# Kernel tuning notes

Measured on AMD Instinct MI355X. Metric: run time of the kernel, lower is better.

The kernel has to match this reference:

```python
import jax, jax.numpy as jnp
import numpy as np
import math

B, DIM, H, W = 16, 384, 64, 64
SCALES, HEADS, HID = 4, 4, 32
WIDTH = DIM // SCALES
NUMS = SCALES - 1
PH = PW = 2
LS = 1e-6


def setup_inputs():
    ks = jax.random.split(jax.random.key(0), 20)
    n = lambda i, shape, s=0.02: jax.random.normal(ks[i], shape, jnp.float32) * s
    return {
        'x': jax.random.normal(ks[0], (B, DIM, H, W), jnp.float32),
        'convs_w': n(1, (NUMS, WIDTH, 3, 3)), 'convs_b': n(2, (NUMS, WIDTH)),
        'pos_w': n(3, (DIM, 2 * HID)), 'pos_b': n(4, (DIM,)),
        'ln_xca_w': jnp.ones((DIM,), jnp.float32), 'ln_xca_b': jnp.zeros((DIM,), jnp.float32),
        'gamma_xca': jnp.full((DIM,), LS, jnp.float32),
        'xca_temp': jnp.ones((HEADS, 1, 1), jnp.float32),
        'xca_kv_w': n(5, (2 * DIM, DIM)), 'xca_kv_b': n(6, (2 * DIM,)),
        'xca_proj_w': n(7, (DIM, DIM)), 'xca_proj_b': n(8, (DIM,)),
        'conv_out_w': n(9, (DIM,)), 'conv_out_b': n(10, (DIM,)),
        'wa_kv_w': n(11, (2 * DIM, DIM)), 'wa_kv_b': n(12, (2 * DIM,)),
        'wa_proj_w': n(13, (DIM, DIM)), 'wa_proj_b': n(14, (DIM,)),
        'ln_w': jnp.ones((DIM,), jnp.float32), 'ln_b': jnp.zeros((DIM,), jnp.float32),
        'pw1_w': n(15, (4 * DIM, DIM)), 'pw1_b': n(16, (4 * DIM,)),
        'pw2_w': n(17, (DIM, 4 * DIM)), 'pw2_b': n(18, (DIM,)),
        'gamma': jnp.full((DIM,), LS, jnp.float32),
    }


def layer_norm(x, w, b, eps=1e-6):
    m = jnp.mean(x, -1, keepdims=True)
    v = jnp.mean((x - m) ** 2, -1, keepdims=True)
    return (x - m) * jax.lax.rsqrt(v + eps) * w + b


def l2norm(x, eps=1e-12):  # torch F.normalize over last dim
    return x / jnp.maximum(jnp.linalg.norm(x, axis=-1, keepdims=True), eps)


def dwconv3x3(x, w, b):  # depthwise: w [Cw,3,3]
    out = jax.lax.conv_general_dilated(x, w[:, None], (1, 1), ((1, 1), (1, 1)),
        dimension_numbers=('NCHW', 'OIHW', 'NCHW'), feature_group_count=w.shape[0])
    return out + b[None, :, None, None]


def pos_fourier(pos_w, pos_b):  # -> [H*W, DIM] (batch-independent since mask is all-false)
    scale = 2 * math.pi
    y = jnp.arange(1, H + 1, dtype=jnp.float32)[:, None] / (H + 1e-6) * scale
    xg = jnp.arange(1, W + 1, dtype=jnp.float32)[None, :] / (W + 1e-6) * scale
    y = jnp.broadcast_to(y, (H, W))
    xg = jnp.broadcast_to(xg, (H, W))
    dim_t = jnp.arange(HID, dtype=jnp.float32)
    dim_t = 10000.0 ** (2 * jnp.floor(dim_t / 2) / HID)
    px = xg[..., None] / dim_t
    py = y[..., None] / dim_t
    px = jnp.stack((jnp.sin(px[..., 0::2]), jnp.cos(px[..., 1::2])), -1).reshape(H, W, HID)
    py = jnp.stack((jnp.sin(py[..., 0::2]), jnp.cos(py[..., 1::2])), -1).reshape(H, W, HID)
    pos = jnp.concatenate((py, px), -1)  # [H,W,2*HID]
    return (pos @ pos_w.T + pos_b).reshape(H * W, DIM)


def xca_fn(x, const, kv_w, kv_b, proj_w, proj_b, temp):
    b, n, c = x.shape
    h, hd = HEADS, c // HEADS
    q1 = const.reshape(b, n, h, hd).transpose(0, 2, 3, 1)          # b,h,hd,n
    kv = (x @ kv_w.T + kv_b).reshape(b, n, 2, h, hd).transpose(2, 0, 3, 1, 4)
    k = l2norm(kv[0].transpose(0, 1, 3, 2))                        # b,h,hd,n (L2 over n)
    v = kv[1].transpose(0, 1, 3, 2)                                # b,h,hd,n
    attn = jax.nn.softmax(jnp.einsum('bhcn,bhdn->bhcd', q1, k) * temp, -1)
    out = jnp.einsum('bhcd,bhdn->bhcn', attn, v)
    out = out.transpose(0, 3, 1, 2).reshape(b, n, c)
    return out @ proj_w.T + proj_b


def window_attn(x, const, kv_w, kv_b, proj_w, proj_b):
    b, n, c = x.shape
    h, hd = HEADS, c // HEADS
    kv = (x @ kv_w.T + kv_b).reshape(b, n, 2, h, hd).transpose(2, 0, 3, 1, 4)
    k = l2norm(kv[0].transpose(0, 1, 3, 2))                        # b,h,hd,n
    v = kv[1].transpose(0, 1, 3, 2)                                # b,h,hd,n
    q1 = const.reshape(b, n, 1, h, hd).transpose(2, 0, 3, 1, 4)    # 1,b,h,n,hd (leading 1 kept, as in torch)
    q1 = q1.transpose(0, 1, 2, 4, 3)                               # 1,b,h,hd,n
    logits = jnp.einsum('obhcn,bhdn->obhcd', q1, k)
    attn = 0.5 * logits / math.sqrt(hd) + 0.5 * jax.nn.softmax(logits, -1)
    attn = jax.nn.softmax(attn, -1)
    out = jnp.einsum('obhcd,bhdn->obhcn', attn, v)                 # 1,b,h,hd,n
    out = out.transpose(0, 2, 1, 3, 4).reshape(b, n, c)            # torch .transpose(1,2).reshape(B,N,C)
    return out @ proj_w.T + proj_b


def unfold(x):  # H,W divisible by patch -> no interpolate branch
    b, c = x.shape[0], x.shape[1]
    nph, npw = H // PH, W // PW
    x = x.reshape(b * c * nph, PH, npw, PW).transpose(0, 2, 1, 3)
    x = x.reshape(b, c, nph * npw, PH * PW).transpose(0, 3, 2, 1)
    return x.reshape(b * PH * PW, nph * npw, c)


def fold(x):
    c = x.shape[-1]
    nph, npw = H // PH, W // PW
    x = x.reshape(B, PH * PW, nph * npw, c).transpose(0, 3, 2, 1)
    x = x.reshape(B * c * nph, npw, PH, PW).transpose(0, 2, 1, 3)
    return x.reshape(B, c, nph * PH, npw * PW)


def reference(x, convs_w, convs_b, pos_w, pos_b, ln_xca_w, ln_xca_b, gamma_xca,
              xca_temp, xca_kv_w, xca_kv_b, xca_proj_w, xca_proj_b,
              conv_out_w, conv_out_b, wa_kv_w, wa_kv_b, wa_proj_w, wa_proj_b,
              ln_w, ln_b, pw1_w, pw1_b, pw2_w, pw2_b, gamma):
    inp = x
    # multi-scale depthwise convs (Res2Net style)
    spx = jnp.split(x, SCALES, axis=1)
    outs = []
    sp = spx[0]
    for i in range(NUMS):
        if i > 0:
            sp = sp + spx[i]
        sp = dwconv3x3(sp, convs_w[i], convs_b[i])
        outs.append(sp)
    x = jnp.concatenate(outs + [spx[NUMS]], axis=1)
    N = H * W
    x3 = x.reshape(B, DIM, N).transpose(0, 2, 1)                   # B,N,C
    x3 = x3 + pos_fourier(pos_w, pos_b)[None]
    const = inp.reshape(B, DIM, N).transpose(0, 2, 1)
    x4 = x3 + gamma_xca * xca_fn(layer_norm(x3, ln_xca_w, ln_xca_b), const,
                                 xca_kv_w, xca_kv_b, xca_proj_w, xca_proj_b, xca_temp)
    x4 = x4.reshape(B, H, W, DIM).transpose(0, 3, 1, 2)
    # conv_out: Conv2d(dim,dim,1,groups=dim) == per-channel scale+bias
    x = x4 * conv_out_w[None, :, None, None] + conv_out_b[None, :, None, None]
    x2 = window_attn(unfold(x), unfold(inp), wa_kv_w, wa_kv_b, wa_proj_w, wa_proj_b)
    x = fold(x2).transpose(0, 2, 3, 1)                             # B,H,W,C
    x = layer_norm(x, ln_w, ln_b)
    x = jax.nn.gelu(x @ pw1_w.T + pw1_b, approximate=False)
    x = x @ pw2_w.T + pw2_b
    x = gamma * x
    return inp + x.transpose(0, 3, 1, 2)
```

## Files before the change

### kernel.cpp

```cpp
#include <hip/hip_runtime.h>
#include <math.h>

#define NBATCH 16
#define CDIM   384
#define NPIX   4096
#define HDCH   96
#define NROWS  65536
#define KVHALF 25165824

typedef unsigned short bf16;
typedef __attribute__((ext_vector_type(8))) short short8;
typedef __attribute__((ext_vector_type(4))) float floatx4;

union S8U { short8 v; bf16 u[8]; };

__device__ __forceinline__ float b2f(bf16 u) {
    union { unsigned int i; float f; } c; c.i = ((unsigned int)u) << 16; return c.f;
}
__device__ __forceinline__ bf16 f2b(float f) {
    union { float f; unsigned int i; } c; c.f = f;
    unsigned int r = (c.i + 0x7FFFu + ((c.i >> 16) & 1u)) >> 16;
    return (bf16)r;
}

__device__ __forceinline__ void gload16(const bf16* g, bf16* l) {
    __builtin_amdgcn_global_load_lds(
        (const __attribute__((address_space(1))) unsigned int*)g,
        (__attribute__((address_space(3))) unsigned int*)l, 16, 0, 0);
}

__global__ __launch_bounds__(256) void zero_kernel(float* __restrict__ p) {
    p[blockIdx.x * 256 + threadIdx.x] = 0.0f;
}

__global__ __launch_bounds__(256) void wcvt_kernel(const float* __restrict__ w,
                                                   bf16* __restrict__ o, int n4) {
    int i = blockIdx.x * 256 + threadIdx.x;
    if (i < n4) {
        float4 v = ((const float4*)w)[i];
        ushort4 u;
        u.x = f2b(v.x); u.y = f2b(v.y); u.z = f2b(v.z); u.w = f2b(v.w);
        ((ushort4*)o)[i] = u;
    }
}

__global__ __launch_bounds__(128) void pos_kernel(const float* __restrict__ pos_w,
                                                  const float* __restrict__ pos_b,
                                                  bf16* __restrict__ pos) {
    __shared__ float feat[64];
    int n = blockIdx.x;
    int yi = n >> 6, xi = n & 63;
    int tid = threadIdx.x;
    if (tid < 64) {
        int j = tid & 31;
        int isx = tid >= 32;
        float base = (float)((isx ? xi : yi) + 1);
        float val = base / (64.0f + 1e-6f) * 6.283185307179586f;
        float e = (float)(2 * (j >> 1)) / 32.0f;
        float dt = powf(10000.0f, e);
        float a = val / dt;
        feat[isx * 32 + j] = (j & 1) ? cosf(a) : sinf(a);
    }
    __syncthreads();
    for (int c = tid; c < CDIM; c += 128) {
        float s = pos_b[c];
        const float* wr = pos_w + c * 64;
        #pragma unroll 16
        for (int j = 0; j < 64; ++j) s += feat[j] * wr[j];
        pos[n * CDIM + c] = f2b(s);
    }
}

__global__ __launch_bounds__(256) void dwconv_kernel(const float* __restrict__ xin, int in_ch0,
                                                     const bf16* __restrict__ prev, int prev_ch0,
                                                     const float* __restrict__ w,
                                                     const float* __restrict__ bias,
                                                     bf16* __restrict__ out, int out_ch0) {
    __shared__ float tile[66][66];
    int b = blockIdx.x / 96, c = blockIdx.x % 96;
    const float* ip = xin + (b * CDIM + in_ch0 + c) * NPIX;
    const bf16* pp = prev ? prev + (b * CDIM + prev_ch0 + c) * NPIX : nullptr;
    int tid = threadIdx.x;
    for (int i = tid; i < 66 * 66; i += 256) {
        int yy = i / 66 - 1, xx = i % 66 - 1;
        float v = 0.0f;
        if (yy >= 0 && yy < 64 && xx >= 0 && xx < 64) {
            v = ip[yy * 64 + xx];
            if (pp) v += b2f(pp[yy * 64 + xx]);
        }
        tile[i / 66][i % 66] = v;
    }
    __syncthreads();
    float wc[9];
    #pragma unroll
    for (int j = 0; j < 9; ++j) wc[j] = w[c * 9 + j];
    float b0 = bias[c];
    bf16* op = out + (b * CDIM + out_ch0 + c) * NPIX;
    for (int p = tid; p < NPIX; p += 256) {
        int y = p >> 6, x = p & 63;
        float a = b0;
        #pragma unroll
        for (int dy = 0; dy < 3; ++dy)
            #pragma unroll
            for (int dx = 0; dx < 3; ++dx)
                a += tile[y + dy][x + dx] * wc[dy * 3 + dx];
        op[p] = f2b(a);
    }
}

__global__ __launch_bounds__(256) void convert_last_kernel(const float* __restrict__ x,
                                                           bf16* __restrict__ xcat) {
    int idx = blockIdx.x * 256 + threadIdx.x;
    int b = idx / (96 * 1024);
    int rem = idx % (96 * 1024);
    const float4* src = (const float4*)(x + (b * CDIM + 288) * NPIX);
    float4 v = src[rem];
    ushort4 o;
    o.x = f2b(v.x); o.y = f2b(v.y); o.z = f2b(v.z); o.w = f2b(v.w);
    ((ushort4*)(xcat + (b * CDIM + 288) * NPIX))[rem] = o;
}

__global__ void x3_kernel(const bf16* __restrict__ xcat, const bf16* __restrict__ pos,
                          bf16* __restrict__ x3) {
    __shared__ float t[32][33];
    int c0 = blockIdx.x * 32, n0 = blockIdx.y * 32, b = blockIdx.z;
    int tx = threadIdx.x, ty = threadIdx.y;
    #pragma unroll
    for (int k = 0; k < 4; ++k) {
        int cl = ty + k * 8;
        t[cl][tx] = b2f(xcat[(b * CDIM + c0 + cl) * NPIX + n0 + tx]);
    }
    __syncthreads();
    #pragma unroll
    for (int k = 0; k < 4; ++k) {
        int nl = ty + k * 8;
        x3[(b * NPIX + n0 + nl) * CDIM + c0 + tx] =
            f2b(t[tx][nl] + b2f(pos[(n0 + nl) * CDIM + c0 + tx]));
    }
}

__global__ __launch_bounds__(128) void ln_kernel(const bf16* __restrict__ in,
                                                 const float* __restrict__ w,
                                                 const float* __restrict__ b,
                                                 bf16* __restrict__ out, int map) {
    int r = blockIdx.x;
    int src = r;
    if (map == 1) {
        int bb = r >> 12;
        int p = r & 4095;
        int y = p >> 6, x = p & 63;
        int patch = ((y & 1) << 1) | (x & 1);
        int blk = ((y >> 1) << 5) | (x >> 1);
        src = ((bb << 2) + patch) * 1024 + blk;
    }
    const bf16* row = in + src * CDIM;
    int tid = threadIdx.x;
    float v[3];
    float s1 = 0.0f, s2 = 0.0f;
    #pragma unroll
    for (int i = 0; i < 3; ++i) {
        v[i] = b2f(row[tid + i * 128]);
        s1 += v[i];
        s2 += v[i] * v[i];
    }
    __shared__ float r1[128], r2[128];
    r1[tid] = s1; r2[tid] = s2;
    __syncthreads();
    for (int off = 64; off > 0; off >>= 1) {
        if (tid < off) { r1[tid] += r1[tid + off]; r2[tid] += r2[tid + off]; }
        __syncthreads();
    }
    float mean = r1[0] * (1.0f / 384.0f);
    float var = fmaxf(r2[0] * (1.0f / 384.0f) - mean * mean, 0.0f);
    float rstd = rsqrtf(var + 1e-6f);
    #pragma unroll
    for (int i = 0; i < 3; ++i) {
        int c = tid + i * 128;
        out[r * CDIM + c] = f2b((v[i] - mean) * rstd * w[c] + b[c]);
    }
}

__global__ __launch_bounds__(256) void mfma_gemm_kernel(const bf16* __restrict__ A,
                                                        const bf16* __restrict__ W,
                                                        const float* __restrict__ bias,
                                                        bf16* __restrict__ C,
                                                        int M, int Nout, int K, int mode,
                                                        const bf16* __restrict__ res,
                                                        const float* __restrict__ scalevec,
                                                        int nlog2,
                                                        float* __restrict__ knsq_out) {
    __shared__ bf16 As[3][128][32];
    __shared__ bf16 Bs[3][128][32];
    int nx = gridDim.x, ny = gridDim.y;
    int d = blockIdx.x + nx * blockIdx.y;
    int nwg = nx * ny;
    int xt, yt;
    if ((nwg & 7) == 0) {
        int cpx = nwg >> 3;
        int wg = (d & 7) * cpx + (d >> 3);
        xt = wg / ny;
        yt = wg % ny;
    } else {
        xt = blockIdx.x; yt = blockIdx.y;
    }
    int m0 = xt * 128;
    int n0 = yt * 128;
    int tid = threadIdx.x;
    int wave = tid >> 6, lane = tid & 63;
    int wm = (wave & 1) * 64;
    int wn = (wave >> 1) * 64;
    int quad = lane >> 4;
    int lrow = lane & 15;

    int p0b = wave * 1024 + lane * 16;
    int o0 = p0b ^ (((p0b >> 7) & 3) << 4);
    int r0 = o0 >> 6;
    int ch0 = (o0 >> 4) & 3;

    const bf16* aSrc0 = A + (size_t)(m0 + r0) * K + ch0 * 8;
    const bf16* aSrc1 = A + (size_t)(m0 + r0 + 64) * K + ch0 * 8;
    const bf16* bSrc0 = W + (size_t)(n0 + r0) * K + ch0 * 8;
    const bf16* bSrc1 = W + (size_t)(n0 + r0 + 64) * K + ch0 * 8;
    bf16* lA0 = &As[0][0][0] + wave * 512;
    bf16* lA1 = &As[0][0][0] + 2048 + wave * 512;
    bf16* lB0 = &Bs[0][0][0] + wave * 512;
    bf16* lB1 = &Bs[0][0][0] + 2048 + wave * 512;

    int rcol = (quad ^ ((lrow >> 1) & 3)) * 8;
    int NT = K >> 5;

#define STAGE(bi_, t_) do { int _off = (bi_) * 4096; int _kk = (t_) * 32; \
        gload16(aSrc0 + _kk, lA0 + _off); \
        gload16(aSrc1 + _kk, lA1 + _off); \
        gload16(bSrc0 + _kk, lB0 + _off); \
        gload16(bSrc1 + _kk, lB1 + _off); } while (0)

    floatx4 acc[4][4] = {};

    STAGE(0, 0);
    STAGE(1, 1);
    asm volatile("s_waitcnt vmcnt(4)" ::: "memory");
    __builtin_amdgcn_s_barrier();
    __builtin_amdgcn_sched_barrier(0);

    for (int t = 0; t < NT; ++t) {
        int bi = t % 3;
        if (t + 2 < NT) STAGE((t + 2) % 3, t + 2);
        short8 af[4], bfr[4];
        #pragma unroll
        for (int i = 0; i < 4; ++i)
            af[i] = *(const short8*)(&As[bi][wm + i * 16 + lrow][rcol]);
        #pragma unroll
        for (int j = 0; j < 4; ++j)
            bfr[j] = *(const short8*)(&Bs[bi][wn + j * 16 + lrow][rcol]);
        #pragma unroll
        for (int i = 0; i < 4; ++i)
            #pragma unroll
            for (int j = 0; j < 4; ++j)
                acc[i][j] = __builtin_amdgcn_mfma_f32_16x16x32_bf16(af[i], bfr[j], acc[i][j], 0, 0, 0);
        if (t + 1 < NT) {
            if (t + 2 < NT) asm volatile("s_waitcnt vmcnt(4)" ::: "memory");
            else            asm volatile("s_waitcnt vmcnt(0)" ::: "memory");
            __builtin_amdgcn_s_barrier();
            __builtin_amdgcn_sched_barrier(0);
        }
    }
#undef STAGE

    if (mode == 3) {
        int nmask = (1 << nlog2) - 1;
        #pragma unroll
        for (int j = 0; j < 4; ++j) {
            int col = n0 + wn + j * 16 + lrow;
            float bv = bias[col];
            if (col < 384) {
                float ss = 0.0f;
                #pragma unroll
                for (int i = 0; i < 4; ++i) {
                    int rowb = m0 + wm + i * 16 + quad * 4;
                    int bb = rowb >> nlog2, tok = rowb & nmask;
                    float v0 = acc[i][j][0] + bv;
                    float v1 = acc[i][j][1] + bv;
                    float v2 = acc[i][j][2] + bv;
                    float v3 = acc[i][j][3] + bv;
                    ss += v0 * v0 + v1 * v1 + v2 * v2 + v3 * v3;
                    ushort4 o;
                    o.x = f2b(v0); o.y = f2b(v1); o.z = f2b(v2); o.w = f2b(v3);
                    *(ushort4*)(C + ((((size_t)bb * 384 + col) << nlog2) | (size_t)tok)) = o;
                }
                int bb0 = (m0 + wm) >> nlog2;
                atomicAdd(&knsq_out[bb0 * CDIM + col], ss);
            } else {
                #pragma unroll
                for (int i = 0; i < 4; ++i) {
                    int rowb = m0 + wm + i * 16 + quad * 4;
                    bf16* vp = C + KVHALF + (size_t)rowb * 384 + (col - 384);
                    #pragma unroll
                    for (int r = 0; r < 4; ++r)
                        vp[(size_t)r * 384] = f2b(acc[i][j][r] + bv);
                }
            }
        }
        return;
    }

    #pragma unroll
    for (int i = 0; i < 4; ++i) {
        int rowb = m0 + wm + i * 16 + quad * 4;
        #pragma unroll
        for (int j = 0; j < 4; ++j) {
            int col = n0 + wn + j * 16 + lrow;
            float bv = bias[col];
            #pragma unroll
            for (int r = 0; r < 4; ++r) {
                int row = rowb + r;
                float v = acc[i][j][r] + bv;
                if (mode == 1) {
                    v = 0.5f * v * (1.0f + erff(v * 0.70710678118654752f));
                } else if (mode == 2) {
                    v = b2f(res[(size_t)row * Nout + col]) + scalevec[col] * v;
                }
                C[(size_t)row * Nout + col] = f2b(v);
            }
        }
    }
}

__global__ __launch_bounds__(256) void chan_qk_mfma(const float* __restrict__ qf,
                                                    const bf16* __restrict__ qb,
                                                    const bf16* __restrict__ KT,
                                                    float* __restrict__ Sg,
                                                    int n_len, int nchunks, int mode) {
    int pair = blockIdx.x / nchunks, ck = blockIdx.x % nchunks;
    int bi = pair >> 2, h = pair & 3;
    int koff = h * HDCH;
    int chunk = n_len / nchunks;
    int nbeg = ck * chunk;
    int tid = threadIdx.x;
    int wave = tid >> 6, lane = tid & 63;
    int lr = lane & 15, q = lane >> 4;
    int c0 = (wave & 1) * 48;
    int d0 = (wave >> 1) * 48;
    floatx4 acc[3][3] = {};
    const size_t qbase = (size_t)(bi * CDIM + koff) * n_len;
    const bf16* kbase = KT + (size_t)(bi * CDIM + koff) * n_len;
    for (int nn = 0; nn < chunk; nn += 32) {
        int n0 = nbeg + nn + q * 8;
        short8 af[3], bfr[3];
        if (mode == 0) {
            #pragma unroll
            for (int i = 0; i < 3; ++i) {
                const float* qp = qf + qbase + (size_t)(c0 + i * 16 + lr) * n_len + n0;
                float4 f0 = *(const float4*)qp;
                float4 f1 = *(const float4*)(qp + 4);
                S8U t;
                t.u[0] = f2b(f0.x); t.u[1] = f2b(f0.y); t.u[2] = f2b(f0.z); t.u[3] = f2b(f0.w);
                t.u[4] = f2b(f1.x); t.u[5] = f2b(f1.y); t.u[6] = f2b(f1.z); t.u[7] = f2b(f1.w);
                af[i] = t.v;
            }
        } else {
            #pragma unroll
            for (int i = 0; i < 3; ++i)
                af[i] = *(const short8*)(qb + qbase + (size_t)(c0 + i * 16 + lr) * n_len + n0);
        }
        #pragma unroll
        for (int j = 0; j < 3; ++j)
            bfr[j] = *(const short8*)(kbase + (size_t)(d0 + j * 16 + lr) * n_len + n0);
        #pragma unroll
        for (int i = 0; i < 3; ++i)
            #pragma unroll
            for (int j = 0; j < 3; ++j)
                acc[i][j] = __builtin_amdgcn_mfma_f32_16x16x32_bf16(af[i], bfr[j], acc[i][j], 0, 0, 0);
    }
    float* Sp = Sg + (size_t)pair * 9216;
    #pragma unroll
    for (int i = 0; i < 3; ++i) {
        int rowb = c0 + i * 16 + q * 4;
        #pragma unroll
        for (int j = 0; j < 3; ++j) {
            int col = d0 + j * 16 + lr;
            #pragma unroll
            for (int r = 0; r < 4; ++r)
                atomicAdd(&Sp[(rowb + r) * 96 + col], acc[i][j][r]);
        }
    }
}

__global__ __launch_bounds__(128) void chan_softmax_kernel(const float* __restrict__ Sg,
                                                           const float* __restrict__ knsq,
                                                           const float* __restrict__ temp,
                                                           bf16* __restrict__ Sb,
                                                           int mode) {
    __shared__ float knrm[96];
    int pair = blockIdx.x;
    int bi = pair >> 2, h = pair & 3;
    int tid = threadIdx.x;
    if (tid < 96)
        knrm[tid] = 1.0f / fmaxf(sqrtf(knsq[bi * CDIM + h * HDCH + tid]), 1e-12f);
    __syncthreads();
    if (tid >= 96) return;
    const float* Sr = Sg + (size_t)pair * 9216 + tid * 96;
    bf16* Ob = Sb + (size_t)pair * 9216 + tid * 96;
    if (mode == 0) {
        float tv = temp[h];
        float m = -1e30f;
        for (int d = 0; d < 96; ++d) m = fmaxf(m, Sr[d] * knrm[d] * tv);
        float s = 0.0f;
        for (int d = 0; d < 96; ++d) s += expf(Sr[d] * knrm[d] * tv - m);
        float inv = 1.0f / s;
        for (int d = 0; d < 96; ++d) Ob[d] = f2b(expf(Sr[d] * knrm[d] * tv - m) * inv);
    } else {
        const float RSQ = 0.10206207261596575f;
        float m1 = -1e30f;
        for (int d = 0; d < 96; ++d) m1 = fmaxf(m1, Sr[d] * knrm[d]);
        float s1 = 0.0f;
        for (int d = 0; d < 96; ++d) s1 += expf(Sr[d] * knrm[d] - m1);
        float inv1 = 1.0f / s1;
        float m2 = -1e30f;
        for (int d = 0; d < 96; ++d) {
            float l = Sr[d] * knrm[d];
            float a = 0.5f * l * RSQ + 0.5f * expf(l - m1) * inv1;
            m2 = fmaxf(m2, a);
        }
        float s2 = 0.0f;
        for (int d = 0; d < 96; ++d) {
            float l = Sr[d] * knrm[d];
            float a = 0.5f * l * RSQ + 0.5f * expf(l - m1) * inv1;
            s2 += expf(a - m2);
        }
        float inv2 = 1.0f / s2;
        for (int d = 0; d < 96; ++d) {
            float l = Sr[d] * knrm[d];
            float a = 0.5f * l * RSQ + 0.5f * expf(l - m1) * inv1;
            Ob[d] = f2b(expf(a - m2) * inv2);
        }
    }
}

#define PVTN 256
__global__ __launch_bounds__(256) void chan_pv_mfma(const bf16* __restrict__ Sb,
                                                    const bf16* __restrict__ V,
                                                    bf16* __restrict__ out,
                                                    int n_len, int mode) {
    int nch = n_len / PVTN;
    int pair = blockIdx.x / nch, ck = blockIdx.x % nch;
    int bi = pair >> 2, h = pair & 3;
    int koff = h * HDCH;
    int tid = threadIdx.x;
    int wave = tid >> 6, lane = tid & 63;
    int lr = lane & 15, q = lane >> 4;
    const bf16* Ab = Sb + (size_t)pair * 9216;
    short8 af[6][3];
    #pragma unroll
    for (int i = 0; i < 6; ++i)
        #pragma unroll
        for (int kt = 0; kt < 3; ++kt)
            af[i][kt] = *(const short8*)(Ab + (i * 16 + lr) * 96 + kt * 32 + q * 8);
    const bf16* vb = V + (size_t)bi * n_len * 384 + koff;
    int nbase = ck * PVTN + wave * 16;
    #pragma unroll
    for (int s = 0; s < 4; ++s) {
        int n = nbase + s * 64 + lr;
        short8 bfr[3];
        #pragma unroll
        for (int kt = 0; kt < 3; ++kt)
            bfr[kt] = *(const short8*)(vb + (size_t)n * 384 + kt * 32 + q * 8);
        floatx4 acc[6] = {};
        #pragma unroll
        for (int kt = 0; kt < 3; ++kt)
            #pragma unroll
            for (int i = 0; i < 6; ++i)
                acc[i] = __builtin_amdgcn_mfma_f32_16x16x32_bf16(af[i][kt], bfr[kt], acc[i], 0, 0, 0);
        if (mode == 0) {
            bf16* op = out + (size_t)(bi * n_len + n) * CDIM + koff;
            #pragma unroll
            for (int i = 0; i < 6; ++i) {
                ushort4 o;
                o.x = f2b(acc[i][0]); o.y = f2b(acc[i][1]);
                o.z = f2b(acc[i][2]); o.w = f2b(acc[i][3]);
                *(ushort4*)(op + i * 16 + q * 4) = o;
            }
        } else {
            #pragma unroll
            for (int i = 0; i < 6; ++i) {
                int cb = i * 16 + q * 4;
                #pragma unroll
                for (int r = 0; r < 4; ++r)
                    out[(size_t)((h * 64 + bi) * HDCH + cb + r) * n_len + n] = f2b(acc[i][r]);
            }
        }
    }
}

__global__ __launch_bounds__(256) void unfold_cu_kernel(const float* __restrict__ xin,
                                                        bf16* __restrict__ cu) {
    int idx = blockIdx.x * 256 + threadIdx.x;
    int b2 = idx / (CDIM * 1024);
    int rem = idx % (CDIM * 1024);
    int ch = rem >> 10, blk = rem & 1023;
    int b = b2 >> 2, patch = b2 & 3;
    int y = ((blk >> 5) << 1) | (patch >> 1);
    int x = ((blk & 31) << 1) | (patch & 1);
    cu[idx] = f2b(xin[(size_t)(b * CDIM + ch) * NPIX + (y << 6) + x]);
}

__global__ __launch_bounds__(256) void unfold_xu_kernel(const bf16* __restrict__ x4,
                                                        const float* __restrict__ cw,
                                                        const float* __restrict__ cb,
                                                        bf16* __restrict__ xu) {
    int idx = blockIdx.x * 256 + threadIdx.x;
    int row = idx / CDIM, ch = idx % CDIM;
    int b2 = row >> 10, blk = row & 1023;
    int b = b2 >> 2, patch = b2 & 3;
    int y = ((blk >> 5) << 1) | (patch >> 1);
    int x = ((blk & 31) << 1) | (patch & 1);
    xu[idx] = f2b(b2f(x4[(size_t)(b * NPIX + (y << 6) + x) * CDIM + ch]) * cw[ch] + cb[ch]);
}

__global__ void out_kernel(const float* __restrict__ xin, const bf16* __restrict__ fin,
                           const float* __restrict__ gamma, float* __restrict__ outp) {
    __shared__ float t[32][33];
    int c0 = blockIdx.x * 32, p0 = blockIdx.y * 32, b = blockIdx.z;
    int tx = threadIdx.x, ty = threadIdx.y;
    #pragma unroll
    for (int k = 0; k < 4; ++k) {
        int pl = ty + k * 8;
        t[pl][tx] = b2f(fin[(size_t)(b * NPIX + p0 + pl) * CDIM + c0 + tx]);
    }
    __syncthreads();
    #pragma unroll
    for (int k = 0; k < 4; ++k) {
        int cl = ty + k * 8;
        size_t addr = (size_t)(b * CDIM + c0 + cl) * NPIX + p0 + tx;
        outp[addr] = xin[addr] + gamma[c0 + cl] * t[tx][cl];
    }
}

extern "C" void kernel_launch(void* const* d_in, const int* in_sizes, int n_in,
                              void* d_out, int out_size, void* d_ws, size_t ws_size,
                              hipStream_t stream) {
    (void)in_sizes; (void)n_in; (void)out_size; (void)ws_size;
    const float* x         = (const float*)d_in[0];
    const float* convs_w   = (const float*)d_in[1];
    const float* convs_b   = (const float*)d_in[2];
    const float* pos_w     = (const float*)d_in[3];
    const float* pos_b     = (const float*)d_in[4];
    const float* ln_xca_w  = (const float*)d_in[5];
    const float* ln_xca_b  = (const float*)d_in[6];
    const float* gamma_xca = (const float*)d_in[7];
    const float* xca_temp  = (const float*)d_in[8];
    const float* xca_kv_w  = (const float*)d_in[9];
    const float* xca_kv_b  = (const float*)d_in[10];
    const float* xca_proj_w= (const float*)d_in[11];
    const float* xca_proj_b= (const float*)d_in[12];
    const float* conv_out_w= (const float*)d_in[13];
    const float* conv_out_b= (const float*)d_in[14];
    const float* wa_kv_w   = (const float*)d_in[15];
    const float* wa_kv_b   = (const float*)d_in[16];
    const float* wa_proj_w = (const float*)d_in[17];
    const float* wa_proj_b = (const float*)d_in[18];
    const float* ln_w      = (const float*)d_in[19];
    const float* ln_b      = (const float*)d_in[20];
    const float* pw1_w     = (const float*)d_in[21];
    const float* pw1_b     = (const float*)d_in[22];
    const float* pw2_w     = (const float*)d_in[23];
    const float* pw2_b     = (const float*)d_in[24];
    const float* gamma     = (const float*)d_in[25];
    float* out = (float*)d_out;

    bf16* pos = (bf16*)d_ws;
    bf16* P1  = pos + 1572864;
    bf16* P2  = P1 + 25165824;
    bf16* P3  = P2 + 25165824;
    float* knsq    = (float*)(P3 + 50331648);
    float* knsq_wa = knsq + 6144;
    float* S_xca   = knsq_wa + 24576;
    float* S_wa    = S_xca + 589824;

    bf16* wbufA = pos + 589824;
    bf16* wbufB = pos;

    zero_kernel<<<11640, 256, 0, stream>>>(knsq);

    pos_kernel<<<4096, 128, 0, stream>>>(pos_w, pos_b, pos);

    dwconv_kernel<<<NBATCH * 96, 256, 0, stream>>>(x,   0, nullptr, 0,  convs_w,        convs_b,       P1, 0);
    dwconv_kernel<<<NBATCH * 96, 256, 0, stream>>>(x,  96, P1,      0,  convs_w + 864,  convs_b + 96,  P1, 96);
    dwconv_kernel<<<NBATCH * 96, 256, 0, stream>>>(x, 192, P1,     96,  convs_w + 1728, convs_b + 192, P1, 192);
    convert_last_kernel<<<6144, 256, 0, stream>>>(x, P1);

    x3_kernel<<<dim3(12, 128, NBATCH), dim3(32, 8), 0, stream>>>(P1, pos, P2);

    ln_kernel<<<NROWS, 128, 0, stream>>>(P2, ln_xca_w, ln_xca_b, P1, 0);
    wcvt_kernel<<<288, 256, 0, stream>>>(xca_kv_w, wbufA, 73728);
    mfma_gemm_kernel<<<dim3(512, 6), 256, 0, stream>>>(P1, wbufA, xca_kv_b, P3,
                                                       NROWS, 768, 384, 3, nullptr, nullptr, 12, knsq);
    chan_qk_mfma<<<512, 256, 0, stream>>>(x, nullptr, P3, S_xca, 4096, 8, 0);
    chan_softmax_kernel<<<64, 128, 0, stream>>>(S_xca, knsq, xca_temp, pos, 0);
    chan_pv_mfma<<<1024, 256, 0, stream>>>(pos, P3 + KVHALF, P1, 4096, 0);
    wcvt_kernel<<<144, 256, 0, stream>>>(xca_proj_w, wbufA, 36864);
    mfma_gemm_kernel<<<dim3(512, 3), 256, 0, stream>>>(P1, wbufA, xca_proj_b, P3,
                                                       NROWS, 384, 384, 2, P2, gamma_xca, 0, nullptr);

    unfold_cu_kernel<<<98304, 256, 0, stream>>>(x, P2);
    unfold_xu_kernel<<<98304, 256, 0, stream>>>(P3, conv_out_w, conv_out_b, P1);
    wcvt_kernel<<<288, 256, 0, stream>>>(wa_kv_w, wbufA, 73728);
    mfma_gemm_kernel<<<dim3(512, 6), 256, 0, stream>>>(P1, wbufA, wa_kv_b, P3,
                                                       NROWS, 768, 384, 3, nullptr, nullptr, 10, knsq_wa);
    chan_qk_mfma<<<512, 256, 0, stream>>>(nullptr, P2, P3, S_wa, 1024, 2, 1);
    chan_softmax_kernel<<<256, 128, 0, stream>>>(S_wa, knsq_wa, nullptr, P2, 1);
    chan_pv_mfma<<<1024, 256, 0, stream>>>(P2, P3 + KVHALF, P1, 1024, 1);
    wcvt_kernel<<<144, 256, 0, stream>>>(wa_proj_w, wbufA, 36864);
    mfma_gemm_kernel<<<dim3(512, 3), 256, 0, stream>>>(P1, wbufA, wa_proj_b, P2,
                                                       NROWS, 384, 384, 0, nullptr, nullptr, 0, nullptr);

    ln_kernel<<<NROWS, 128, 0, stream>>>(P2, ln_w, ln_b, P1, 1);
    wcvt_kernel<<<576, 256, 0, stream>>>(pw1_w, wbufA, 147456);
    wcvt_kernel<<<576, 256, 0, stream>>>(pw2_w, wbufB, 147456);
    for (int ch = 0; ch < 2; ++ch) {
        mfma_gemm_kernel<<<dim3(256, 12), 256, 0, stream>>>(P1 + (size_t)ch * 32768 * 384, wbufA, pw1_b,
                                                            P3, 32768, 1536, 384, 1, nullptr, nullptr, 0, nullptr);
        mfma_gemm_kernel<<<dim3(256, 3), 256, 0, stream>>>(P3, wbufB, pw2_b,
                                                           P2 + (size_t)ch * 32768 * 384, 32768, 384, 1536,
                                                           0, nullptr, nullptr, 0, nullptr);
    }

    out_kernel<<<dim3(12, 128, NBATCH), dim3(32, 8), 0, stream>>>(x, P2, gamma, out);
}
```

Before: 1.263 ms.

## Fold conv_out into window-attn KV weights and unfold via GEMM A-row remap

Removes the separate unfold_xu pass. The per-channel conv_out scale is folded into the wa_kv weight conversion, and its bias is folded into a precomputed KV bias. The KV GEMM now reads rows of the x4 tensor through an unfold index remap on its A-operand loads. This drops a full read and write of a large bf16 activation. Separately, the exact erf GELU in the pw1 GEMM epilogue is replaced with the tanh-form approximation computed through exp, which is cheaper but changes numerics slightly.

```diff
diff --git a/kernel.cpp b/kernel.cpp
--- a/kernel.cpp
+++ b/kernel.cpp
@@ -27,6 +27,14 @@
     __builtin_amdgcn_global_load_lds(
         (const __attribute__((address_space(1))) unsigned int*)g,
         (__attribute__((address_space(3))) unsigned int*)l, 16, 0, 0);
+}
+
+__device__ __forceinline__ int unfold_src(int r) {
+    int b2 = r >> 10, blk = r & 1023;
+    int b = b2 >> 2, patch = b2 & 3;
+    int y = ((blk >> 5) << 1) | (patch >> 1);
+    int x = ((blk & 31) << 1) | (patch & 1);
+    return b * NPIX + (y << 6) + x;
 }
 
 __global__ __launch_bounds__(256) void zero_kernel(float* __restrict__ p) {
@@ -41,6 +49,34 @@
         ushort4 u;
         u.x = f2b(v.x); u.y = f2b(v.y); u.z = f2b(v.z); u.w = f2b(v.w);
         ((ushort4*)o)[i] = u;
+    }
+}
+
+__global__ __launch_bounds__(256) void wcvt_scale_kernel(const float* __restrict__ w,
+                                                         const float* __restrict__ cw,
+                                                         bf16* __restrict__ o, int n4) {
+    int i = blockIdx.x * 256 + threadIdx.x;
+    if (i < n4) {
+        float4 v = ((const float4*)w)[i];
+        float4 s = ((const float4*)cw)[i % 96];
+        ushort4 u;
+        u.x = f2b(v.x * s.x); u.y = f2b(v.y * s.y);
+        u.z = f2b(v.z * s.z); u.w = f2b(v.w * s.w);
+        ((ushort4*)o)[i] = u;
+    }
+}
+
+__global__ __launch_bounds__(256) void biasfold_kernel(const float* __restrict__ w,
+                                                       const float* __restrict__ b,
+                                                       const float* __restrict__ cb,
+                                                       float* __restrict__ o) {
+    int col = blockIdx.x * 256 + threadIdx.x;
+    if (col < 768) {
+        float s = b[col];
+        const float* wr = w + col * 384;
+        #pragma unroll 8
+        for (int k = 0; k < 384; ++k) s += wr[k] * cb[k];
+        o[col] = s;
     }
 }
 
@@ -183,12 +219,13 @@
 __global__ __launch_bounds__(256) void mfma_gemm_kernel(const bf16* __restrict__ A,
                                                         const bf16* __restrict__ W,
                                                         const float* __restrict__ bias,
-                                                        bf16* __restrict__ C,
+                                                        bf16* C,
                                                         int M, int Nout, int K, int mode,
-                                                        const bf16* __restrict__ res,
+                                                        const bf16* res,
                                                         const float* __restrict__ scalevec,
                                                         int nlog2,
-                                                        float* __restrict__ knsq_out) {
+                                                        float* __restrict__ knsq_out,
+                                                        int aremap) {
     __shared__ bf16 As[3][128][32];
     __shared__ bf16 Bs[3][128][32];
     int nx = gridDim.x, ny = gridDim.y;
@@ -217,8 +254,10 @@
     int r0 = o0 >> 6;
     int ch0 = (o0 >> 4) & 3;
 
-    const bf16* aSrc0 = A + (size_t)(m0 + r0) * K + ch0 * 8;
-    const bf16* aSrc1 = A + (size_t)(m0 + r0 + 64) * K + ch0 * 8;
+    int ar0 = m0 + r0, ar1 = m0 + r0 + 64;
+    if (aremap) { ar0 = unfold_src(ar0); ar1 = unfold_src(ar1); }
+    const bf16* aSrc0 = A + (size_t)ar0 * K + ch0 * 8;
+    const bf16* aSrc1 = A + (size_t)ar1 * K + ch0 * 8;
     const bf16* bSrc0 = W + (size_t)(n0 + r0) * K + ch0 * 8;
     const bf16* bSrc1 = W + (size_t)(n0 + r0 + 64) * K + ch0 * 8;
     bf16* lA0 = &As[0][0][0] + wave * 512;
@@ -316,7 +355,8 @@
                 int row = rowb + r;
                 float v = acc[i][j][r] + bv;
                 if (mode == 1) {
-                    v = 0.5f * v * (1.0f + erff(v * 0.70710678118654752f));
+                    float t = __expf(-1.5957691216057308f * (v + 0.044715f * v * v * v));
+                    v = v / (1.0f + t);
                 } else if (mode == 2) {
                     v = b2f(res[(size_t)row * Nout + col]) + scalevec[col] * v;
                 }
@@ -504,19 +544,6 @@
     cu[idx] = f2b(xin[(size_t)(b * CDIM + ch) * NPIX + (y << 6) + x]);
 }
 
-__global__ __launch_bounds__(256) void unfold_xu_kernel(const bf16* __restrict__ x4,
-                                                        const float* __restrict__ cw,
-                                                        const float* __restrict__ cb,
-                                                        bf16* __restrict__ xu) {
-    int idx = blockIdx.x * 256 + threadIdx.x;
-    int row = idx / CDIM, ch = idx % CDIM;
-    int b2 = row >> 10, blk = row & 1023;
-    int b = b2 >> 2, patch = b2 & 3;
-    int y = ((blk >> 5) << 1) | (patch >> 1);
-    int x = ((blk & 31) << 1) | (patch & 1);
-    xu[idx] = f2b(b2f(x4[(size_t)(b * NPIX + (y << 6) + x) * CDIM + ch]) * cw[ch] + cb[ch]);
-}
-
 __global__ void out_kernel(const float* __restrict__ xin, const bf16* __restrict__ fin,
                            const float* __restrict__ gamma, float* __restrict__ outp) {
     __shared__ float t[32][33];
@@ -579,6 +606,7 @@
 
     bf16* wbufA = pos + 589824;
     bf16* wbufB = pos;
+    float* bias_wa = S_xca;
 
     zero_kernel<<<11640, 256, 0, stream>>>(knsq);
 
@@ -594,35 +622,35 @@
     ln_kernel<<<NROWS, 128, 0, stream>>>(P2, ln_xca_w, ln_xca_b, P1, 0);
     wcvt_kernel<<<288, 256, 0, stream>>>(xca_kv_w, wbufA, 73728);
     mfma_gemm_kernel<<<dim3(512, 6), 256, 0, stream>>>(P1, wbufA, xca_kv_b, P3,
-                                                       NROWS, 768, 384, 3, nullptr, nullptr, 12, knsq);
+                                                       NROWS, 768, 384, 3, nullptr, nullptr, 12, knsq, 0);
     chan_qk_mfma<<<512, 256, 0, stream>>>(x, nullptr, P3, S_xca, 4096, 8, 0);
     chan_softmax_kernel<<<64, 128, 0, stream>>>(S_xca, knsq, xca_temp, pos, 0);
     chan_pv_mfma<<<1024, 256, 0, stream>>>(pos, P3 + KVHALF, P1, 4096, 0);
     wcvt_kernel<<<144, 256, 0, stream>>>(xca_proj_w, wbufA, 36864);
-    mfma_gemm_kernel<<<dim3(512, 3), 256, 0, stream>>>(P1, wbufA, xca_proj_b, P3,
-                                                       NROWS, 384, 384, 2, P2, gamma_xca, 0, nullptr);
-
-    unfold_cu_kernel<<<98304, 256, 0, stream>>>(x, P2);
-    unfold_xu_kernel<<<98304, 256, 0, stream>>>(P3, conv_out_w, conv_out_b, P1);
-    wcvt_kernel<<<288, 256, 0, stream>>>(wa_kv_w, wbufA, 73728);
-    mfma_gemm_kernel<<<dim3(512, 6), 256, 0, stream>>>(P1, wbufA, wa_kv_b, P3,
-                                                       NROWS, 768, 384, 3, nullptr, nullptr, 10, knsq_wa);
-    chan_qk_mfma<<<512, 256, 0, stream>>>(nullptr, P2, P3, S_wa, 1024, 2, 1);
+    mfma_gemm_kernel<<<dim3(512, 3), 256, 0, stream>>>(P1, wbufA, xca_proj_b, P2,
+                                                       NROWS, 384, 384, 2, P2, gamma_xca, 0, nullptr, 0);
+
+    biasfold_kernel<<<3, 256, 0, stream>>>(wa_kv_w, wa_kv_b, conv_out_b, bias_wa);
+    wcvt_scale_kernel<<<288, 256, 0, stream>>>(wa_kv_w, conv_out_w, wbufA, 73728);
+    mfma_gemm_kernel<<<dim3(512, 6), 256, 0, stream>>>(P2, wbufA, bias_wa, P3,
+                                                       NROWS, 768, 384, 3, nullptr, nullptr, 10, knsq_wa, 1);
+    unfold_cu_kernel<<<98304, 256, 0, stream>>>(x, P1);
+    chan_qk_mfma<<<512, 256, 0, stream>>>(nullptr, P1, P3, S_wa, 1024, 2, 1);
     chan_softmax_kernel<<<256, 128, 0, stream>>>(S_wa, knsq_wa, nullptr, P2, 1);
     chan_pv_mfma<<<1024, 256, 0, stream>>>(P2, P3 + KVHALF, P1, 1024, 1);
     wcvt_kernel<<<144, 256, 0, stream>>>(wa_proj_w, wbufA, 36864);
     mfma_gemm_kernel<<<dim3(512, 3), 256, 0, stream>>>(P1, wbufA, wa_proj_b, P2,
-                                                       NROWS, 384, 384, 0, nullptr, nullptr, 0, nullptr);
+                                                       NROWS, 384, 384, 0, nullptr, nullptr, 0, nullptr, 0);
 
     ln_kernel<<<NROWS, 128, 0, stream>>>(P2, ln_w, ln_b, P1, 1);
     wcvt_kernel<<<576, 256, 0, stream>>>(pw1_w, wbufA, 147456);
     wcvt_kernel<<<576, 256, 0, stream>>>(pw2_w, wbufB, 147456);
     for (int ch = 0; ch < 2; ++ch) {
         mfma_gemm_kernel<<<dim3(256, 12), 256, 0, stream>>>(P1 + (size_t)ch * 32768 * 384, wbufA, pw1_b,
-                                                            P3, 32768, 1536, 384, 1, nullptr, nullptr, 0, nullptr);
+                                                            P3, 32768, 1536, 384, 1, nullptr, nullptr, 0, nullptr, 0);
         mfma_gemm_kernel<<<dim3(256, 3), 256, 0, stream>>>(P3, wbufB, pw2_b,
                                                            P2 + (size_t)ch * 32768 * 384, 32768, 384, 1536,
-                                                           0, nullptr, nullptr, 0, nullptr);
+                                                           0, nullptr, nullptr, 0, nullptr, 0);
     }
 
     out_kernel<<<dim3(12, 128, NBATCH), dim3(32, 8), 0, stream>>>(x, P2, gamma, out);
```

After: 1.242 ms. Within noise of the previous version (-1.7%).
